# Optimization experiments

Measured on AMD Instinct MI355X. Metric: run time of the kernel, lower is better.

The kernel has to match this reference:

```python
import jax, jax.numpy as jnp
import numpy as np

HEADS = 16
DIM_HEAD = 64
SCALE = DIM_HEAD ** -0.5


def setup_inputs() -> dict:
    key = jax.random.key(0)
    k1, k2, k3 = jax.random.split(key, 3)
    B, N, D = 4, 8192, 1024
    inner = HEADS * DIM_HEAD  # 1024
    x = jax.random.normal(k1, (B, N, D), dtype=jnp.float32)
    w_qkv = jax.random.normal(k2, (D, 3 * inner), dtype=jnp.float32) * (D ** -0.5)
    w_out = jax.random.normal(k3, (inner, D), dtype=jnp.float32) * (inner ** -0.5)
    b_out = jnp.zeros((D,), dtype=jnp.float32)
    return {"x": x, "w_qkv": w_qkv, "w_out": w_out, "b_out": b_out}


def reference(x, w_qkv, w_out, b_out):
    B, N, D = x.shape
    h, d = HEADS, DIM_HEAD
    qkv = x @ w_qkv  # [B, N, 3*h*d]
    q, k, v = jnp.split(qkv, 3, axis=-1)

    def to_heads(t):  # b n (h d) -> (b h) n d
        return t.reshape(B, N, h, d).transpose(0, 2, 1, 3).reshape(B * h, N, d)

    q, k, v = map(to_heads, (q, k, v))
    q = jax.nn.softmax(q * SCALE, axis=-1)   # softmax over feature dim
    k = jax.nn.softmax(k, axis=-2)           # softmax over sequence dim
    # context = q^T k per head: [bh, d, e]
    context = jnp.einsum('bnd,bne->bde', q, k)
    # out[b,n,e] = sum_d context[b,d,e] * v[b,n,d]
    out = jnp.einsum('bde,bnd->bne', context, v)
    out = out.reshape(B, h, N, d).transpose(0, 2, 1, 3).reshape(B, N, h * d)
    return out @ w_out + b_out
```

## Files before the change

kernel.cpp:

```cpp
#include <hip/hip_runtime.h>

typedef unsigned short u16;
typedef __attribute__((ext_vector_type(8))) short short8;
typedef __attribute__((ext_vector_type(4))) unsigned short u16x4;
typedef __attribute__((ext_vector_type(8))) __bf16 bf16x8;
typedef __attribute__((ext_vector_type(4))) float f32x4;

#define B_SZ 4
#define NSEQ 8192
#define DMODEL 1024
#define MROWS 32768
#define QKVCOLS 3072

static __device__ __forceinline__ u16 f2bf(float f) {
  unsigned u = __builtin_bit_cast(unsigned, f);
  u += 0x7fffu + ((u >> 16) & 1u);
  return (u16)(u >> 16);
}
static __device__ __forceinline__ float bf2f(u16 h) {
  return __builtin_bit_cast(float, ((unsigned)h) << 16);
}
static __device__ __forceinline__ void gload16(const u16* g, u16* l) {
  __builtin_amdgcn_global_load_lds(
      (const __attribute__((address_space(1))) unsigned*)g,
      (__attribute__((address_space(3))) unsigned*)l, 16, 0, 0);
}

__global__ __launch_bounds__(256) void k_convert(const float* __restrict__ in,
                                                 u16* __restrict__ out, long n) {
  long i = ((long)blockIdx.x * 256 + threadIdx.x) * 4;
  if (i >= n) return;
  f32x4 v = *(const f32x4*)(in + i);
  u16x4 o;
  o[0] = f2bf(v[0]); o[1] = f2bf(v[1]); o[2] = f2bf(v[2]); o[3] = f2bf(v[3]);
  *(u16x4*)(out + i) = o;
}

__global__ __launch_bounds__(256) void k_transpose(const float* __restrict__ in,
                                                   u16* __restrict__ out, int R, int C) {
  __shared__ float tile[32][33];
  int c0 = blockIdx.x * 32, r0 = blockIdx.y * 32;
  int tx = threadIdx.x, ty = threadIdx.y;
#pragma unroll
  for (int j = 0; j < 32; j += 8)
    tile[ty + j][tx] = in[(long)(r0 + ty + j) * C + c0 + tx];
  __syncthreads();
#pragma unroll
  for (int j = 0; j < 32; j += 8)
    out[(long)(c0 + ty + j) * R + r0 + tx] = f2bf(tile[tx][ty + j]);
}

#define MFMA_QUAD(Qm, Qn, A_, B_)                                              \
  _Pragma("unroll") for (int m = 0; m < 4; ++m)                                \
  _Pragma("unroll") for (int n = 0; n < 2; ++n)                                \
    acc[Qm][Qn][m][n] = __builtin_amdgcn_mfma_f32_16x16x32_bf16(A_[m][1], B_[n][1], \
        __builtin_amdgcn_mfma_f32_16x16x32_bf16(A_[m][0], B_[n][0], acc[Qm][Qn][m][n], 0, 0, 0), 0, 0, 0);

template <int EPI, int K, int LDA, int NBN, int LDC, long BSTR>
__global__ __launch_bounds__(512, 2) void k_gemm256(
    const u16* __restrict__ A, const u16* __restrict__ Bp,
    const float* __restrict__ bias, u16* __restrict__ qh,
    u16* __restrict__ kh, u16* __restrict__ vh,
    float* __restrict__ Cf, float* __restrict__ S) {
  __shared__ __align__(16) u16 sm[65536];
  const int t = threadIdx.x;
  const int lane = t & 63;
  const int w = t >> 6;
  const int wq = w >> 2;
  const int wn = w & 3;
  const int lr = lane & 15;
  const int hi = lane >> 4;
  const int l3 = lane >> 3;

  const int nwg = gridDim.x;
  const int bid = blockIdx.x;
  const int swz = (bid & 7) * (nwg >> 3) + (bid >> 3);
  const int per = 8 * NBN;
  const int grp = swz / per, rem = swz % per;
  const int bm = grp * 8 + (rem & 7);
  const int bn = rem / 8;

  const u16* B = Bp + (long)(bm >> 5) * BSTR;
  const int gcol = ((lane & 7) ^ l3) * 8;

  auto stA = [&](int tile, int half, int buf) {
    u16* dst = &sm[buf * 16384 + (half * 128 + w * 16) * 64];
    const u16* g = A + ((long)(bm * 256 + half * 128 + w * 16 + l3)) * LDA + tile * 64 + gcol;
    gload16(g, dst);
    gload16(g + 8 * (long)LDA, dst + 8 * 64);
  };
  auto stB = [&](int tile, int half, int buf) {
#pragma unroll
    for (int L = 0; L < 2; ++L) {
      int base = half * 128 + w * 16 + L * 8;
      int grow = bn * 256 + ((base >> 5) & 3) * 64 + half * 32 + (base & 31) + l3;
      const u16* g = B + (long)grow * K + tile * 64 + gcol;
      gload16(g, &sm[32768 + buf * 16384 + base * 64]);
    }
  };

  const int su = (lr & 7) << 3;
  const int cu0 = (hi * 8) ^ su;
  const int cu1 = (32 + hi * 8) ^ su;
  const int arow = wq * 64 + lr;
  const int brow = wn * 32 + lr;

  auto ldA = [&](int buf, int Qm, int m, int kk) -> bf16x8 {
    return *(const bf16x8*)&sm[buf * 16384 + (Qm * 128 + arow + m * 16) * 64 + (kk ? cu1 : cu0)];
  };
  auto ldB = [&](int buf, int Qn, int n, int kk) -> bf16x8 {
    return *(const bf16x8*)&sm[32768 + buf * 16384 + (Qn * 128 + brow + n * 16) * 64 + (kk ? cu1 : cu0)];
  };

  f32x4 acc[2][2][4][2] = {};
  bf16x8 af[4][2], af2[4][2], bl[2][2], bh[2][2];
  constexpr int NT = K >> 6;

  stA(0, 0, 0); stB(0, 0, 0); stB(0, 1, 0); stA(0, 1, 0);
  stA(1, 0, 1); stB(1, 0, 1); stB(1, 1, 1);
  asm volatile("s_waitcnt vmcnt(6)" ::: "memory");
  __builtin_amdgcn_s_barrier();

  auto tile_body = [&](int tt, int s1, int s2) {
    const int p = tt & 1;
#pragma unroll
    for (int m = 0; m < 4; ++m) { af[m][0] = ldA(p, 0, m, 0); af[m][1] = ldA(p, 0, m, 1); }
#pragma unroll
    for (int n = 0; n < 2; ++n) { bl[n][0] = ldB(p, 0, n, 0); bl[n][1] = ldB(p, 0, n, 1); }
    __builtin_amdgcn_sched_barrier(0);
#pragma unroll
    for (int n = 0; n < 2; ++n) { bh[n][0] = ldB(p, 1, n, 0); bh[n][1] = ldB(p, 1, n, 1); }
    __builtin_amdgcn_sched_barrier(0);
    if (s1) stA(tt + 1, 1, 1 - p);
    __builtin_amdgcn_sched_barrier(0);
    asm volatile("s_waitcnt lgkmcnt(4)" ::: "memory");
    __builtin_amdgcn_sched_barrier(0);
    __builtin_amdgcn_s_setprio(1);
    MFMA_QUAD(0, 0, af, bl)
    __builtin_amdgcn_s_setprio(0);
    __builtin_amdgcn_s_barrier();
#pragma unroll
    for (int m = 0; m < 4; ++m) { af2[m][0] = ldA(p, 1, m, 0); af2[m][1] = ldA(p, 1, m, 1); }
    __builtin_amdgcn_sched_barrier(0);
    if (s2) stA(tt + 2, 0, p);
    __builtin_amdgcn_sched_barrier(0);
    asm volatile("s_waitcnt lgkmcnt(8)" ::: "memory");
    __builtin_amdgcn_sched_barrier(0);
    __builtin_amdgcn_s_setprio(1);
    MFMA_QUAD(0, 1, af, bh)
    __builtin_amdgcn_s_setprio(0);
    __builtin_amdgcn_s_barrier();
    if (s2) { stB(tt + 2, 0, p); stB(tt + 2, 1, p); }
    __builtin_amdgcn_sched_barrier(0);
    asm volatile("s_waitcnt lgkmcnt(0)" ::: "memory");
    __builtin_amdgcn_sched_barrier(0);
    __builtin_amdgcn_s_setprio(1);
    MFMA_QUAD(1, 1, af2, bh)
    MFMA_QUAD(1, 0, af2, bl)
    __builtin_amdgcn_s_setprio(0);
    if (s2) { asm volatile("s_waitcnt vmcnt(6)" ::: "memory"); }
    else if (s1) { asm volatile("s_waitcnt vmcnt(0)" ::: "memory"); }
    __builtin_amdgcn_s_barrier();
  };

  for (int tt = 0; tt < NT - 2; ++tt) tile_body(tt, 1, 1);
  tile_body(NT - 2, 1, 0);
  tile_body(NT - 1, 0, 0);

  const int row0 = bm * 256 + wq * 64 + hi * 4;
  const int colw = bn * 256 + wn * 64;

  if (EPI == 1) {
#pragma unroll
    for (int Qm = 0; Qm < 2; ++Qm)
#pragma unroll
      for (int m = 0; m < 4; ++m)
#pragma unroll
        for (int r = 0; r < 4; ++r) {
          long row = row0 + Qm * 128 + m * 16 + r;
#pragma unroll
          for (int Qn = 0; Qn < 2; ++Qn)
#pragma unroll
            for (int n = 0; n < 2; ++n) {
              int col = colw + Qn * 32 + n * 16 + lr;
              Cf[row * LDC + col] = acc[Qm][Qn][m][n][r] + bias[col];
            }
        }
    return;
  }

  if (bn < 4) {
    const int h = bn * 4 + wn;
#pragma unroll
    for (int Qm = 0; Qm < 2; ++Qm)
#pragma unroll
      for (int m = 0; m < 4; ++m)
#pragma unroll
        for (int r = 0; r < 4; ++r) {
          float pv[2][2];
          float mx = -1e30f;
#pragma unroll
          for (int Qn = 0; Qn < 2; ++Qn)
#pragma unroll
            for (int nn = 0; nn < 2; ++nn) {
              pv[Qn][nn] = acc[Qm][Qn][m][nn][r] * 0.125f;
              mx = fmaxf(mx, pv[Qn][nn]);
            }
#pragma unroll
          for (int off = 1; off < 16; off <<= 1) mx = fmaxf(mx, __shfl_xor(mx, off));
          float s = 0.f;
#pragma unroll
          for (int Qn = 0; Qn < 2; ++Qn)
#pragma unroll
            for (int nn = 0; nn < 2; ++nn) { pv[Qn][nn] = __expf(pv[Qn][nn] - mx); s += pv[Qn][nn]; }
#pragma unroll
          for (int off = 1; off < 16; off <<= 1) s += __shfl_xor(s, off);
          float inv = 1.0f / s;
          long row = row0 + Qm * 128 + m * 16 + r;
          long base = (((long)(row >> 13) * 16 + h) * NSEQ + (row & 8191)) * 64;
#pragma unroll
          for (int Qn = 0; Qn < 2; ++Qn)
#pragma unroll
            for (int nn = 0; nn < 2; ++nn)
              qh[base + Qn * 32 + nn * 16 + lr] = f2bf(pv[Qn][nn] * inv);
        }
  } else if (bn < 8) {
    const int h = (bn - 4) * 4 + wn;
    float cs[2][2] = {};
#pragma unroll
    for (int Qm = 0; Qm < 2; ++Qm)
#pragma unroll
      for (int m = 0; m < 4; ++m)
#pragma unroll
        for (int r = 0; r < 4; ++r) {
          long row = row0 + Qm * 128 + m * 16 + r;
          long base = (((long)(row >> 13) * 16 + h) * NSEQ + (row & 8191)) * 64;
#pragma unroll
          for (int Qn = 0; Qn < 2; ++Qn)
#pragma unroll
            for (int nn = 0; nn < 2; ++nn) {
              float pe = __expf(acc[Qm][Qn][m][nn][r]);
              cs[Qn][nn] += pe;
              kh[base + Qn * 32 + nn * 16 + lr] = f2bf(pe);
            }
        }
#pragma unroll
    for (int Qn = 0; Qn < 2; ++Qn)
#pragma unroll
      for (int nn = 0; nn < 2; ++nn) {
        cs[Qn][nn] += __shfl_xor(cs[Qn][nn], 16);
        cs[Qn][nn] += __shfl_xor(cs[Qn][nn], 32);
      }
    if (lane < 16) {
      int b = bm >> 5;
#pragma unroll
      for (int Qn = 0; Qn < 2; ++Qn)
#pragma unroll
        for (int nn = 0; nn < 2; ++nn)
          atomicAdd(&S[b * DMODEL + h * 64 + Qn * 32 + nn * 16 + lane], cs[Qn][nn]);
    }
  } else {
    const int vcol = (bn - 8) * 256 + wn * 64;
#pragma unroll
    for (int Qm = 0; Qm < 2; ++Qm)
#pragma unroll
      for (int m = 0; m < 4; ++m)
#pragma unroll
        for (int r = 0; r < 4; ++r) {
          long row = row0 + Qm * 128 + m * 16 + r;
#pragma unroll
          for (int Qn = 0; Qn < 2; ++Qn)
#pragma unroll
            for (int nn = 0; nn < 2; ++nn)
              vh[row * DMODEL + vcol + Qn * 32 + nn * 16 + lr] = f2bf(acc[Qm][Qn][m][nn][r]);
        }
  }
}

__global__ __launch_bounds__(256) void k_ctx(const u16* __restrict__ qhat,
                                             const u16* __restrict__ khat,
                                             float* __restrict__ ctx_part) {
  __shared__ __align__(16) u16 smu[2 * 17408];
  const int bh = blockIdx.x, nc = blockIdx.y;
  const int t = threadIdx.x;
  const int lane = t & 63;
  const int ww = t >> 6;
  const int lr = lane & 15;
  const int hi = lane >> 4;

  const int isK = t >> 7;
  const int u = t & 127;
  const int ng = u >> 3;
  const int dc = u & 7;
  const u16* srcm = (isK ? khat : qhat) + (long)bh * NSEQ * 64;

  f32x4 acc[4][4] = {};
  short8 v[8];

  auto load_stage = [&](int s) {
    long nb = (long)nc * 1024 + s * 128;
    const u16* src = srcm + (nb + ng * 8) * 64 + dc * 8;
#pragma unroll
    for (int i = 0; i < 8; ++i) v[i] = *(const short8*)(src + i * 64);
  };
  auto write_stage = [&](int s) {
    const int buf = s & 1;
    u16* dst0 = &smu[buf * 17408 + isK * 8704 + (dc * 8) * 136 + (ng ^ dc) * 8];
#pragma unroll
    for (int j = 0; j < 8; ++j) {
      short8 o;
#pragma unroll
      for (int i = 0; i < 8; ++i) o[i] = v[i][j];
      *(short8*)(dst0 + j * 136) = o;
    }
  };
  auto compute = [&](int s) {
    const int buf = s & 1;
    const int g = ww * 4 + hi;
    const u16* qb = &smu[buf * 17408];
    const u16* kb = qb + 8704;
    bf16x8 a[4], b[4];
#pragma unroll
    for (int dt = 0; dt < 4; ++dt) {
      int d = dt * 16 + lr;
      a[dt] = *(const bf16x8*)(qb + d * 136 + (g ^ ((d >> 3) & 7)) * 8);
    }
#pragma unroll
    for (int et = 0; et < 4; ++et) {
      int d = et * 16 + lr;
      b[et] = *(const bf16x8*)(kb + d * 136 + (g ^ ((d >> 3) & 7)) * 8);
    }
#pragma unroll
    for (int dt = 0; dt < 4; ++dt)
#pragma unroll
      for (int et = 0; et < 4; ++et)
        acc[dt][et] = __builtin_amdgcn_mfma_f32_16x16x32_bf16(a[dt], b[et], acc[dt][et], 0, 0, 0);
  };

  load_stage(0);
  write_stage(0);
  __syncthreads();
  for (int s = 0; s < 8; ++s) {
    if (s < 7) load_stage(s + 1);
    compute(s);
    if (s < 7) write_stage(s + 1);
    __syncthreads();
  }

  float* smf = (float*)smu;
#pragma unroll
  for (int dt = 0; dt < 4; ++dt)
#pragma unroll
    for (int et = 0; et < 4; ++et)
      *(f32x4*)&smf[ww * 4096 + (dt * 4 + hi) * 256 + (et * 16 + lr) * 4] = acc[dt][et];
  __syncthreads();
  float* op = ctx_part + ((long)nc * 64 + bh) * 4096;
#pragma unroll
  for (int rep = 0; rep < 4; ++rep) {
    int p4 = rep * 1024 + t * 4;
    f32x4 sum = *(const f32x4*)&smf[p4];
    sum += *(const f32x4*)&smf[4096 + p4];
    sum += *(const f32x4*)&smf[8192 + p4];
    sum += *(const f32x4*)&smf[12288 + p4];
    *(f32x4*)&op[p4] = sum;
  }
}

__global__ __launch_bounds__(256) void k_cred(const float* __restrict__ ctx_part,
                                              float* __restrict__ ctx) {
  const int bh = blockIdx.x;
  const int p = blockIdx.y * 256 + threadIdx.x;
  float s = 0.f;
#pragma unroll
  for (int nc = 0; nc < 8; ++nc)
    s += ctx_part[((long)nc * 64 + bh) * 4096 + p];
  int d = (p >> 8) * 4 + (p & 3);
  int e = (p >> 2) & 63;
  ctx[(long)bh * 4096 + d * 64 + e] = s;
}

__global__ __launch_bounds__(256) void k_w2(const float* __restrict__ ctx,
                                            const float* __restrict__ S,
                                            const u16* __restrict__ woutT,
                                            u16* __restrict__ w2t) {
  __shared__ float cl[64][68];
  const int b = blockIdx.x, h = blockIdx.y, ec = blockIdx.z;
  const float* cp = ctx + ((long)(b * 16 + h)) * 4096;
  const float* Sp = S + b * DMODEL + h * 64;
  for (int i = threadIdx.x; i < 4096; i += 256) {
    int d = i >> 6, e = i & 63;
    cl[d][e] = cp[i] / Sp[e];
  }
  __syncthreads();
  const int eo = ec * 128 + (threadIdx.x & 127);
  const int dg = (threadIdx.x >> 7) * 32;
  const u16* wp = woutT + (long)eo * DMODEL + h * 64;
  float wv[64];
#pragma unroll
  for (int j = 0; j < 8; ++j) {
    short8 v8 = *(const short8*)(wp + j * 8);
#pragma unroll
    for (int i = 0; i < 8; ++i) wv[j * 8 + i] = bf2f((u16)v8[i]);
  }
  f32x4 w4[16];
#pragma unroll
  for (int j = 0; j < 16; ++j) w4[j] = *(const f32x4*)&wv[j * 4];
  u16* outp = w2t + ((long)b << 20) + (long)eo * DMODEL + h * 64;
  for (int d = dg; d < dg + 32; ++d) {
    f32x4 a = {0.f, 0.f, 0.f, 0.f};
#pragma unroll
    for (int j = 0; j < 16; ++j) {
      f32x4 c4 = *(const f32x4*)&cl[d][j * 4];
      a += c4 * w4[j];
    }
    outp[d] = f2bf(a[0] + a[1] + a[2] + a[3]);
  }
}

extern "C" void kernel_launch(void* const* d_in, const int* in_sizes, int n_in,
                              void* d_out, int out_size, void* d_ws, size_t ws_size,
                              hipStream_t stream) {
  const float* x = (const float*)d_in[0];
  const float* w_qkv = (const float*)d_in[1];
  const float* w_out = (const float*)d_in[2];
  const float* b_out = (const float*)d_in[3];
  float* out = (float*)d_out;
  char* ws = (char*)d_ws;

  u16* xb      = (u16*)(ws + 0);
  u16* wqkvT   = (u16*)(ws + 67108864L);
  u16* woutT   = (u16*)(ws + 73400320L);
  u16* qhat    = (u16*)(ws + 75497472L);
  u16* khat    = (u16*)(ws + 142606336L);
  u16* vhat    = (u16*)(ws + 209715200L);
  u16* w2t     = (u16*)(ws + 276824064L);
  float* S     = (float*)(ws + 285212672L);
  float* ctx   = (float*)(ws + 285229056L);
  float* cpart = (float*)(ws + 286277632L);

  hipMemsetAsync(S, 0, 16384, stream);

  k_convert<<<32768, 256, 0, stream>>>(x, xb, (long)MROWS * DMODEL);
  k_transpose<<<dim3(96, 32), dim3(32, 8), 0, stream>>>(w_qkv, wqkvT, DMODEL, QKVCOLS);
  k_transpose<<<dim3(32, 32), dim3(32, 8), 0, stream>>>(w_out, woutT, DMODEL, DMODEL);

  k_gemm256<0, DMODEL, DMODEL, 12, QKVCOLS, 0L>
      <<<dim3((MROWS / 256) * (QKVCOLS / 256)), 512, 0, stream>>>(
      xb, wqkvT, nullptr, qhat, khat, vhat, nullptr, S);

  k_ctx<<<dim3(64, 8), 256, 0, stream>>>(qhat, khat, cpart);
  k_cred<<<dim3(64, 16), 256, 0, stream>>>(cpart, ctx);
  k_w2<<<dim3(4, 16, 8), 256, 0, stream>>>(ctx, S, woutT, w2t);

  k_gemm256<1, DMODEL, DMODEL, 4, DMODEL, (long)DMODEL * DMODEL>
      <<<dim3((MROWS / 256) * (DMODEL / 256)), 512, 0, stream>>>(
      vhat, w2t, b_out, nullptr, nullptr, nullptr, out, nullptr);
}
```

Baseline: 390.1 us.

## Fold V projection into output weight so final GEMM reads x directly

Stops materialising V in the QKV GEMM, which now computes only Q and K columns. Instead it forms a per-batch combined weight (W_v · context · W_out) with two small MFMA kernels, and the final GEMM multiplies the bf16 input x by that combined weight. This drops a third of the big QKV GEMM and the V write and read, in exchange for extra small weight-combining GEMMs and another rounding to bf16 of the combined weight.

```diff
diff --git a/kernel.cpp b/kernel.cpp
--- a/kernel.cpp
+++ b/kernel.cpp
@@ -36,6 +36,16 @@
   *(u16x4*)(out + i) = o;
 }
 
+__global__ __launch_bounds__(256) void k_cv(const float* __restrict__ wq,
+                                            u16* __restrict__ wvb) {
+  int idx = (blockIdx.x * 256 + threadIdx.x) * 4;
+  int i = idx >> 10, k = idx & 1023;
+  f32x4 v = *(const f32x4*)(wq + (long)i * QKVCOLS + 2048 + k);
+  u16x4 o;
+  o[0] = f2bf(v[0]); o[1] = f2bf(v[1]); o[2] = f2bf(v[2]); o[3] = f2bf(v[3]);
+  *(u16x4*)(wvb + idx) = o;
+}
+
 __global__ __launch_bounds__(256) void k_transpose(const float* __restrict__ in,
                                                    u16* __restrict__ out, int R, int C) {
   __shared__ float tile[32][33];
@@ -60,8 +70,7 @@
 __global__ __launch_bounds__(512, 2) void k_gemm256(
     const u16* __restrict__ A, const u16* __restrict__ Bp,
     const float* __restrict__ bias, u16* __restrict__ qh,
-    u16* __restrict__ kh, u16* __restrict__ vh,
-    float* __restrict__ Cf, float* __restrict__ S) {
+    u16* __restrict__ kh, float* __restrict__ Cf, float* __restrict__ S) {
   __shared__ __align__(16) u16 sm[65536];
   const int t = threadIdx.x;
   const int lane = t & 63;
@@ -224,7 +233,7 @@
             for (int nn = 0; nn < 2; ++nn)
               qh[base + Qn * 32 + nn * 16 + lr] = f2bf(pv[Qn][nn] * inv);
         }
-  } else if (bn < 8) {
+  } else {
     const int h = (bn - 4) * 4 + wn;
     float cs[2][2] = {};
 #pragma unroll
@@ -259,21 +268,6 @@
         for (int nn = 0; nn < 2; ++nn)
           atomicAdd(&S[b * DMODEL + h * 64 + Qn * 32 + nn * 16 + lane], cs[Qn][nn]);
     }
-  } else {
-    const int vcol = (bn - 8) * 256 + wn * 64;
-#pragma unroll
-    for (int Qm = 0; Qm < 2; ++Qm)
-#pragma unroll
-      for (int m = 0; m < 4; ++m)
-#pragma unroll
-        for (int r = 0; r < 4; ++r) {
-          long row = row0 + Qm * 128 + m * 16 + r;
-#pragma unroll
-          for (int Qn = 0; Qn < 2; ++Qn)
-#pragma unroll
-            for (int nn = 0; nn < 2; ++nn)
-              vh[row * DMODEL + vcol + Qn * 32 + nn * 16 + lr] = f2bf(acc[Qm][Qn][m][nn][r]);
-        }
   }
 }
 
@@ -367,8 +361,10 @@
 }
 
 __global__ __launch_bounds__(256) void k_cred(const float* __restrict__ ctx_part,
-                                              float* __restrict__ ctx) {
+                                              const float* __restrict__ S,
+                                              u16* __restrict__ ctxn) {
   const int bh = blockIdx.x;
+  const int b = bh >> 4, h = bh & 15;
   const int p = blockIdx.y * 256 + threadIdx.x;
   float s = 0.f;
 #pragma unroll
@@ -376,45 +372,105 @@
     s += ctx_part[((long)nc * 64 + bh) * 4096 + p];
   int d = (p >> 8) * 4 + (p & 3);
   int e = (p >> 2) & 63;
-  ctx[(long)bh * 4096 + d * 64 + e] = s;
-}
-
-__global__ __launch_bounds__(256) void k_w2(const float* __restrict__ ctx,
-                                            const float* __restrict__ S,
-                                            const u16* __restrict__ woutT,
-                                            u16* __restrict__ w2t) {
-  __shared__ float cl[64][68];
-  const int b = blockIdx.x, h = blockIdx.y, ec = blockIdx.z;
-  const float* cp = ctx + ((long)(b * 16 + h)) * 4096;
-  const float* Sp = S + b * DMODEL + h * 64;
-  for (int i = threadIdx.x; i < 4096; i += 256) {
-    int d = i >> 6, e = i & 63;
-    cl[d][e] = cp[i] / Sp[e];
+  ctxn[(long)bh * 4096 + d * 64 + e] = f2bf(s / S[b * DMODEL + h * 64 + e]);
+}
+
+__global__ __launch_bounds__(256) void k_ct(const u16* __restrict__ woutT,
+                                            const u16* __restrict__ ctxn,
+                                            u16* __restrict__ ctT) {
+  __shared__ __align__(16) u16 cb[64 * 72];
+  const int b = blockIdx.x, h = blockIdx.y;
+  const int t = threadIdx.x, lane = t & 63, ww = t >> 6;
+  const int lr = lane & 15, hi = lane >> 4;
+  {
+    const u16* src = ctxn + ((long)(b * 16 + h)) * 4096 + t * 16;
+    int row = t >> 2, col = (t & 3) * 16;
+    *(short8*)(cb + row * 72 + col) = *(const short8*)src;
+    *(short8*)(cb + row * 72 + col + 8) = *(const short8*)(src + 8);
   }
   __syncthreads();
-  const int eo = ec * 128 + (threadIdx.x & 127);
-  const int dg = (threadIdx.x >> 7) * 32;
-  const u16* wp = woutT + (long)eo * DMODEL + h * 64;
-  float wv[64];
-#pragma unroll
-  for (int j = 0; j < 8; ++j) {
-    short8 v8 = *(const short8*)(wp + j * 8);
-#pragma unroll
-    for (int i = 0; i < 8; ++i) wv[j * 8 + i] = bf2f((u16)v8[i]);
-  }
-  f32x4 w4[16];
-#pragma unroll
-  for (int j = 0; j < 16; ++j) w4[j] = *(const f32x4*)&wv[j * 4];
-  u16* outp = w2t + ((long)b << 20) + (long)eo * DMODEL + h * 64;
-  for (int d = dg; d < dg + 32; ++d) {
-    f32x4 a = {0.f, 0.f, 0.f, 0.f};
-#pragma unroll
-    for (int j = 0; j < 16; ++j) {
-      f32x4 c4 = *(const f32x4*)&cl[d][j * 4];
-      a += c4 * w4[j];
-    }
-    outp[d] = f2bf(a[0] + a[1] + a[2] + a[3]);
-  }
+  bf16x8 bfrag[4][2];
+#pragma unroll
+  for (int n = 0; n < 4; ++n)
+#pragma unroll
+    for (int kk = 0; kk < 2; ++kk)
+      bfrag[n][kk] = *(const bf16x8*)(cb + (n * 16 + lr) * 72 + kk * 32 + hi * 8);
+  const int row0 = ww * 256;
+  u16* outp = ctT + ((long)b * 1024) * 1024 + (long)h * 64;
+#pragma unroll
+  for (int m = 0; m < 16; ++m) {
+    int arow = row0 + m * 16 + lr;
+    const u16* ap = woutT + (long)arow * DMODEL + h * 64;
+    bf16x8 a0 = *(const bf16x8*)(ap + hi * 8);
+    bf16x8 a1 = *(const bf16x8*)(ap + 32 + hi * 8);
+    f32x4 accr[4] = {};
+#pragma unroll
+    for (int n = 0; n < 4; ++n)
+      accr[n] = __builtin_amdgcn_mfma_f32_16x16x32_bf16(a1, bfrag[n][1],
+                __builtin_amdgcn_mfma_f32_16x16x32_bf16(a0, bfrag[n][0], accr[n], 0, 0, 0), 0, 0, 0);
+#pragma unroll
+    for (int n = 0; n < 4; ++n)
+#pragma unroll
+      for (int r = 0; r < 4; ++r)
+        outp[(long)(row0 + m * 16 + hi * 4 + r) * DMODEL + n * 16 + lr] = f2bf(accr[n][r]);
+  }
+}
+
+__global__ __launch_bounds__(256) void k_wc(const u16* __restrict__ A,
+                                            const u16* __restrict__ B,
+                                            u16* __restrict__ Cb) {
+  __shared__ __align__(16) u16 As[128 * 32];
+  __shared__ __align__(16) u16 Bs[128 * 32];
+  const int K = 1024, ldc = 1024;
+  const int t = threadIdx.x;
+  const int lane = t & 63;
+  const int w = t >> 6;
+  const int wm = w >> 1, wn = w & 1;
+  const long bm = blockIdx.x, bn = blockIdx.y;
+
+  f32x4 acc[4][4] = {};
+
+  const u16* Ag = A + bm * 128 * (long)K;
+  const u16* Bg = B + bn * 128 * (long)K;
+  const int r0 = t >> 2;
+  const int s0 = (t & 3) * 8;
+  const int ko = (lane >> 4) * 8;
+  const int lr = lane & 15;
+
+  for (int kt = 0; kt < K; kt += 32) {
+    short8 a0 = *(const short8*)(Ag + (long)r0 * K + kt + s0);
+    short8 a1 = *(const short8*)(Ag + (long)(r0 + 64) * K + kt + s0);
+    short8 b0 = *(const short8*)(Bg + (long)r0 * K + kt + s0);
+    short8 b1 = *(const short8*)(Bg + (long)(r0 + 64) * K + kt + s0);
+    __syncthreads();
+    *(short8*)(As + r0 * 32 + s0) = a0;
+    *(short8*)(As + (r0 + 64) * 32 + s0) = a1;
+    *(short8*)(Bs + r0 * 32 + s0) = b0;
+    *(short8*)(Bs + (r0 + 64) * 32 + s0) = b1;
+    __syncthreads();
+    bf16x8 af[4], bfr[4];
+#pragma unroll
+    for (int m = 0; m < 4; ++m)
+      af[m] = *(const bf16x8*)(As + (wm * 64 + m * 16 + lr) * 32 + ko);
+#pragma unroll
+    for (int n = 0; n < 4; ++n)
+      bfr[n] = *(const bf16x8*)(Bs + (wn * 64 + n * 16 + lr) * 32 + ko);
+#pragma unroll
+    for (int m = 0; m < 4; ++m)
+#pragma unroll
+      for (int n = 0; n < 4; ++n)
+        acc[m][n] = __builtin_amdgcn_mfma_f32_16x16x32_bf16(af[m], bfr[n], acc[m][n], 0, 0, 0);
+  }
+
+  const int row_base = (int)bm * 128 + wm * 64 + (lane >> 4) * 4;
+  const int col_base = (int)bn * 128 + wn * 64 + lr;
+#pragma unroll
+  for (int m = 0; m < 4; ++m)
+#pragma unroll
+    for (int n = 0; n < 4; ++n)
+#pragma unroll
+      for (int r = 0; r < 4; ++r)
+        Cb[(long)(row_base + m * 16 + r) * ldc + col_base + n * 16] = f2bf(acc[m][n][r]);
 }
 
 extern "C" void kernel_launch(void* const* d_in, const int* in_sizes, int n_in,
@@ -430,29 +486,32 @@
   u16* xb      = (u16*)(ws + 0);
   u16* wqkvT   = (u16*)(ws + 67108864L);
   u16* woutT   = (u16*)(ws + 73400320L);
-  u16* qhat    = (u16*)(ws + 75497472L);
-  u16* khat    = (u16*)(ws + 142606336L);
-  u16* vhat    = (u16*)(ws + 209715200L);
-  u16* w2t     = (u16*)(ws + 276824064L);
-  float* S     = (float*)(ws + 285212672L);
-  float* ctx   = (float*)(ws + 285229056L);
-  float* cpart = (float*)(ws + 286277632L);
+  u16* wvb     = (u16*)(ws + 75497472L);
+  u16* qhat    = (u16*)(ws + 77594624L);
+  u16* khat    = (u16*)(ws + 144703488L);
+  float* S     = (float*)(ws + 211812352L);
+  u16* ctxn    = (u16*)(ws + 211828736L);
+  float* cpart = (float*)(ws + 212353024L);
+  u16* ctT     = (u16*)(ws + 220741632L);
+  u16* wcT     = (u16*)(ws + 229130240L);
 
   hipMemsetAsync(S, 0, 16384, stream);
 
   k_convert<<<32768, 256, 0, stream>>>(x, xb, (long)MROWS * DMODEL);
-  k_transpose<<<dim3(96, 32), dim3(32, 8), 0, stream>>>(w_qkv, wqkvT, DMODEL, QKVCOLS);
+  k_cv<<<1024, 256, 0, stream>>>(w_qkv, wvb);
+  k_transpose<<<dim3(64, 32), dim3(32, 8), 0, stream>>>(w_qkv, wqkvT, DMODEL, QKVCOLS);
   k_transpose<<<dim3(32, 32), dim3(32, 8), 0, stream>>>(w_out, woutT, DMODEL, DMODEL);
 
-  k_gemm256<0, DMODEL, DMODEL, 12, QKVCOLS, 0L>
-      <<<dim3((MROWS / 256) * (QKVCOLS / 256)), 512, 0, stream>>>(
-      xb, wqkvT, nullptr, qhat, khat, vhat, nullptr, S);
+  k_gemm256<0, DMODEL, DMODEL, 8, QKVCOLS, 0L>
+      <<<dim3((MROWS / 256) * (2048 / 256)), 512, 0, stream>>>(
+      xb, wqkvT, nullptr, qhat, khat, nullptr, S);
 
   k_ctx<<<dim3(64, 8), 256, 0, stream>>>(qhat, khat, cpart);
-  k_cred<<<dim3(64, 16), 256, 0, stream>>>(cpart, ctx);
-  k_w2<<<dim3(4, 16, 8), 256, 0, stream>>>(ctx, S, woutT, w2t);
+  k_cred<<<dim3(64, 16), 256, 0, stream>>>(cpart, S, ctxn);
+  k_ct<<<dim3(4, 16), 256, 0, stream>>>(woutT, ctxn, ctT);
+  k_wc<<<dim3(32, 8), 256, 0, stream>>>(ctT, wvb, wcT);
 
   k_gemm256<1, DMODEL, DMODEL, 4, DMODEL, (long)DMODEL * DMODEL>
       <<<dim3((MROWS / 256) * (DMODEL / 256)), 512, 0, stream>>>(
-      vhat, w2t, b_out, nullptr, nullptr, nullptr, out, nullptr);
-}
+      xb, wcT, b_out, nullptr, nullptr, out, nullptr);
+}
```

Measured after the change: 331.8 us, median of 2. 1.18x faster.
